# Optimization experiments

Measured on AMD Instinct MI355X. Metric: run time of the kernel, lower is better.

Reference implementation:

```python
import jax, jax.numpy as jnp
import numpy as np

B, S, D, H = 2, 2048, 2048, 16
HD = D // H  # head_dim = 128


def setup_inputs() -> dict:
    key = jax.random.key(0)
    k1, k2, k3, k4, k5, k6 = jax.random.split(key, 6)
    scale = 1.0 / np.sqrt(D)
    return {
        "hidden_states": jax.random.normal(k1, (B, S, D), dtype=jnp.float32),
        "attention_mask": jnp.ones((B, S), dtype=jnp.int32),
        "wq": jax.random.normal(k2, (D, D), dtype=jnp.float32) * scale,
        "wk": jax.random.normal(k3, (D, D), dtype=jnp.float32) * scale,
        "wv": jax.random.normal(k4, (D, D), dtype=jnp.float32) * scale,
        "wo": jax.random.normal(k5, (D, D), dtype=jnp.float32) * scale,
        "bo": jax.random.normal(k6, (D,), dtype=jnp.float32) * 0.01,
    }


def reference(hidden_states, attention_mask, wq, wk, wv, wo, bo):
    b, s, d = hidden_states.shape
    # QKV projections (no bias), split heads -> [B, S, H, HD]
    q = (hidden_states @ wq).reshape(b, s, H, HD)
    k = (hidden_states @ wk).reshape(b, s, H, HD)
    v = (hidden_states @ wv).reshape(b, s, H, HD)

    # combined causal + padding mask -> [B, 1, S, S]
    causal = jnp.tril(jnp.ones((s, s), dtype=bool))[None, None]
    pad = (attention_mask > 0)[:, None, None, :]  # [B,1,1,S]
    mask = jnp.logical_and(causal, pad)

    big_neg = jnp.finfo(hidden_states.dtype).min
    bias = jnp.where(mask, 0.0, big_neg).astype(hidden_states.dtype)

    # scaled dot-product attention (flax dot_product_attention scales by 1/sqrt(head_dim))
    scores = jnp.einsum("bqhd,bkhd->bhqk", q, k) / jnp.sqrt(jnp.asarray(HD, hidden_states.dtype))
    probs = jax.nn.softmax(scores + bias, axis=-1)
    ctx = jnp.einsum("bhqk,bkhd->bqhd", probs, v).reshape(b, s, d)

    return ctx @ wo + bo
```

## Files before the change

### kernel.cpp

```cpp
#include <hip/hip_runtime.h>
#include <hip/hip_bf16.h>
#include <stdint.h>

#define Bv 2
#define Sv 2048
#define Dv 2048
#define Hv 16
#define HDv 128
#define Mv (Bv*Sv)

typedef __attribute__((ext_vector_type(8))) short short8;
typedef __attribute__((ext_vector_type(4))) short short4v;
typedef __attribute__((ext_vector_type(4))) float f32x4;

__device__ __forceinline__ unsigned short bf16_rne(float f) {
    union { float f; uint32_t u; } c; c.f = f;
    uint32_t u = c.u;
    u += 0x7fffu + ((u >> 16) & 1u);
    return (unsigned short)(u >> 16);
}

__device__ __forceinline__ uint32_t cvt_pk_bf16(float lo, float hi) {
    uint32_t r;
    asm("v_cvt_pk_bf16_f32 %0, %1, %2" : "=v"(r) : "v"(lo), "v"(hi));
    return r;
}

__device__ __forceinline__ void gload16(const void* g, void* l) {
    __builtin_amdgcn_global_load_lds((const __attribute__((address_space(1))) void*)g,
                                     (__attribute__((address_space(3))) void*)l, 16, 0, 0);
}

__global__ void cvt_x_kernel(const float* __restrict__ x, unsigned short* __restrict__ xb) {
    int i = (blockIdx.x * 256 + threadIdx.x) * 4;
    float4 v = *(const float4*)(x + i);
    short4v o;
    o[0] = (short)bf16_rne(v.x);
    o[1] = (short)bf16_rne(v.y);
    o[2] = (short)bf16_rne(v.z);
    o[3] = (short)bf16_rne(v.w);
    *(short4v*)(xb + i) = o;
}

__global__ void cvt_wt_kernel(const float* __restrict__ w0, const float* __restrict__ w1,
                              const float* __restrict__ w2, const float* __restrict__ w3,
                              unsigned short* __restrict__ wt) {
    __shared__ unsigned short t[64][65];
    int z = blockIdx.z;
    const float* w = (z == 0) ? w0 : (z == 1) ? w1 : (z == 2) ? w2 : w3;
    unsigned short* o = wt + (size_t)z * Dv * Dv;
    int k0 = blockIdx.x * 64, n0 = blockIdx.y * 64;
    for (int i = threadIdx.x; i < 4096; i += 256) {
        int r = i >> 6, c = i & 63;
        t[r][c] = bf16_rne(w[(size_t)(k0 + r) * Dv + n0 + c]);
    }
    __syncthreads();
    for (int i = threadIdx.x; i < 4096; i += 256) {
        int r = i >> 6, c = i & 63;
        o[(size_t)(n0 + r) * Dv + k0 + c] = t[c][r];
    }
}

template<int FOUT>
__global__ __launch_bounds__(256) void gemm_bt_kernel(
    const unsigned short* __restrict__ A,
    const unsigned short* __restrict__ WtBase,
    unsigned short* __restrict__ CbBase,
    unsigned short* __restrict__ VTout,
    float* __restrict__ Cf,
    const float* __restrict__ bias)
{
    __shared__ unsigned short lA[128 * 32];
    __shared__ unsigned short lB[128 * 32];
    const int tid = threadIdx.x;
    const int wv = tid >> 6, ln = tid & 63;
    const int lr = ln & 15, lg = ln >> 4;
    const int wm = wv >> 1, wn = wv & 1;
    const int m0 = blockIdx.x * 128, n0 = blockIdx.y * 128;
    const int z = blockIdx.z;
    const unsigned short* Wt = WtBase + (size_t)z * Dv * Dv;
    unsigned short* Cb = CbBase + (size_t)z * (size_t)Mv * Dv;

    const int srow = tid >> 2;
    const int scol = (tid & 3) * 8;

    f32x4 acc[4][4];
    #pragma unroll
    for (int m = 0; m < 4; m++)
        #pragma unroll
        for (int n = 0; n < 4; n++)
            acc[m][n] = (f32x4){0.f, 0.f, 0.f, 0.f};

    for (int kt = 0; kt < Dv; kt += 32) {
        gload16(A  + (size_t)(m0 +      srow) * Dv + kt + scol, &lA[wv * 512]);
        gload16(A  + (size_t)(m0 + 64 + srow) * Dv + kt + scol, &lA[2048 + wv * 512]);
        gload16(Wt + (size_t)(n0 +      srow) * Dv + kt + scol, &lB[wv * 512]);
        gload16(Wt + (size_t)(n0 + 64 + srow) * Dv + kt + scol, &lB[2048 + wv * 512]);
        __syncthreads();

        short8 af[4], bfv[4];
        #pragma unroll
        for (int m = 0; m < 4; m++)
            af[m] = *(const short8*)&lA[(wm * 64 + m * 16 + lr) * 32 + lg * 8];
        #pragma unroll
        for (int n = 0; n < 4; n++)
            bfv[n] = *(const short8*)&lB[(wn * 64 + n * 16 + lr) * 32 + lg * 8];
        #pragma unroll
        for (int m = 0; m < 4; m++)
            #pragma unroll
            for (int n = 0; n < 4; n++)
                acc[m][n] = __builtin_amdgcn_mfma_f32_16x16x32_bf16(af[m], bfv[n], acc[m][n], 0, 0, 0);
        __syncthreads();
    }

    #pragma unroll
    for (int m = 0; m < 4; m++) {
        #pragma unroll
        for (int n = 0; n < 4; n++) {
            int row = m0 + wm * 64 + m * 16 + lg * 4;
            int col = n0 + wn * 64 + n * 16 + lr;
            if (FOUT) {
                #pragma unroll
                for (int r = 0; r < 4; r++)
                    Cf[(size_t)(row + r) * Dv + col] = acc[m][n][r] + bias[col];
            } else if (z == 2) {
                int bb = row >> 11, s = row & (Sv - 1);
                short4v o;
                #pragma unroll
                for (int r = 0; r < 4; r++) o[r] = (short)bf16_rne(acc[m][n][r]);
                *(short4v*)&VTout[((size_t)bb * Dv + col) * Sv + s] = o;
            } else {
                #pragma unroll
                for (int r = 0; r < 4; r++)
                    Cb[(size_t)(row + r) * Dv + col] = bf16_rne(acc[m][n][r]);
            }
        }
    }
}

__global__ __launch_bounds__(512) void attn_kernel(
    const unsigned short* __restrict__ Q, const unsigned short* __restrict__ K,
    const unsigned short* __restrict__ VT, const int* __restrict__ pmask,
    unsigned short* __restrict__ CTX)
{
    __shared__ unsigned short lK[2][64 * 128];
    __shared__ unsigned short lVt[2][128 * 64];
    __shared__ int lPmB[2][64];
    __shared__ int lPmOk[2];

    const int tid = threadIdx.x, wv = tid >> 6, ln = tid & 63;
    const int lr = ln & 15, lg = ln >> 4;
    const int L = blockIdx.x;
    const int bh = (L & 7) * 4 + ((L >> 3) & 3);
    const int b = bh >> 4, h = bh & 15;
    const int v = L >> 5;
    const int qidx = (v < 8) ? (15 - v) : (v - 8);
    const int q0 = qidx * 128;
    const int qw0 = q0 + wv * 16;
    const size_t hoff  = (size_t)b * Sv * Dv + (size_t)h * HDv;
    const size_t vtoff = ((size_t)b * Dv + (size_t)h * HDv) * Sv;

    short8 qf[4];
    #pragma unroll
    for (int ds = 0; ds < 4; ds++)
        qf[ds] = *(const short8*)&Q[hoff + (size_t)(qw0 + lr) * Dv + ds * 32 + lg * 8];

    size_t koff[2], voff[2];
    #pragma unroll
    for (int ii = 0; ii < 2; ++ii) {
        int slot = ii * 512 + wv * 64 + ln;
        int krow = slot >> 4, kch = slot & 15;
        koff[ii] = hoff + (size_t)krow * Dv + ((kch ^ (krow & 7)) << 3);
        int vrow = slot >> 3, vch = slot & 7;
        voff[ii] = vtoff + (size_t)vrow * Sv + ((vch ^ (vrow & 7)) << 3);
    }

    auto STAGE = [&](int t, int buf) {
        const size_t kadd = (size_t)(t << 6) * Dv;
        const int vadd = t << 6;
        unsigned short* kb = &lK[buf][0];
        unsigned short* vb = &lVt[buf][0];
        #pragma unroll
        for (int ii = 0; ii < 2; ++ii) {
            gload16(K + koff[ii] + kadd, kb + (ii * 512 + wv * 64) * 8);
            gload16(VT + voff[ii] + vadd, vb + (ii * 512 + wv * 64) * 8);
        }
        if (wv == 0) {
            int pmv = pmask[b * Sv + (t << 6) + ln];
            lPmB[buf][ln] = pmv;
            unsigned long long bal = __ballot(pmv != 0);
            if (ln == 0) lPmOk[buf] = (bal == ~0ull) ? 1 : 0;
        }
    };

    f32x4 acc[8];
    #pragma unroll
    for (int n = 0; n < 8; n++) acc[n] = (f32x4){0.f, 0.f, 0.f, 0.f};
    float mrow = -3.0e38f, lrow = 0.f;
    const float CS = 0.12751744f;
    const int qg = qw0 + lr;
    const int nt = (q0 >> 6) + 2;
    const int srcA = lr + ((lg & 1) << 5);
    const int srcB = srcA + 16;
    const bool hiSel = (lg >= 2);

    auto TILE = [&](int t, int buf, auto CAUSAL_c) {
        constexpr bool CAUSAL = decltype(CAUSAL_c)::value;
        const int kv0 = t << 6;
        const unsigned short* kb = &lK[buf][0];
        const unsigned short* vb = &lVt[buf][0];

        f32x4 st[4];
        #pragma unroll
        for (int t2 = 0; t2 < 4; ++t2) st[t2] = (f32x4){0.f, 0.f, 0.f, 0.f};
        __builtin_amdgcn_s_setprio(1);
        #pragma unroll
        for (int t2 = 0; t2 < 4; ++t2) {
            const int krow = t2 * 16 + lr;
            #pragma unroll
            for (int ds = 0; ds < 4; ++ds) {
                const int ch = ds * 4 + lg;
                short8 kf = *(const short8*)&kb[krow * 128 + ((ch ^ (krow & 7)) << 3)];
                st[t2] = __builtin_amdgcn_mfma_f32_16x16x32_bf16(kf, qf[ds], st[t2], 0, 0, 0);
            }
        }
        __builtin_amdgcn_s_setprio(0);

        float sv[4][4];
        float rmax;
        if constexpr (CAUSAL) {
            const int* pm = &lPmB[buf][0];
            #pragma unroll
            for (int t2 = 0; t2 < 4; ++t2)
                #pragma unroll
                for (int r = 0; r < 4; ++r) {
                    int kvl = t2 * 16 + lg * 4 + r;
                    bool ok = ((kv0 + kvl) <= qg) && (pm[kvl] != 0);
                    sv[t2][r] = ok ? st[t2][r] * CS : -1.0e30f;
                }
            rmax = sv[0][0];
            #pragma unroll
            for (int t2 = 0; t2 < 4; ++t2)
                #pragma unroll
                for (int r = 0; r < 4; ++r) rmax = fmaxf(rmax, sv[t2][r]);
            rmax = fmaxf(rmax, __shfl_xor(rmax, 16, 64));
            rmax = fmaxf(rmax, __shfl_xor(rmax, 32, 64));
        } else {
            rmax = st[0][0];
            #pragma unroll
            for (int t2 = 0; t2 < 4; ++t2)
                #pragma unroll
                for (int r = 0; r < 4; ++r) rmax = fmaxf(rmax, st[t2][r]);
            rmax = fmaxf(rmax, __shfl_xor(rmax, 16, 64));
            rmax = fmaxf(rmax, __shfl_xor(rmax, 32, 64));
            rmax *= CS;
        }

        if (!__all(rmax - mrow <= 8.0f)) {
            float mn = fmaxf(mrow, rmax);
            float alpha = exp2f(mrow - mn);
            mrow = mn;
            lrow *= alpha;
            #pragma unroll
            for (int n = 0; n < 8; n++)
                #pragma unroll
                for (int r = 0; r < 4; r++) acc[n][r] *= alpha;
        }

        float p[4][4]; float psum = 0.f;
        if constexpr (CAUSAL) {
            #pragma unroll
            for (int t2 = 0; t2 < 4; ++t2)
                #pragma unroll
                for (int r = 0; r < 4; ++r) {
                    float e = exp2f(sv[t2][r] - mrow);
                    p[t2][r] = (sv[t2][r] > -5.0e29f) ? e : 0.f;
                    psum += p[t2][r];
                }
        } else {
            if (lPmOk[buf]) {
                #pragma unroll
                for (int t2 = 0; t2 < 4; ++t2)
                    #pragma unroll
                    for (int r = 0; r < 4; ++r) {
                        p[t2][r] = exp2f(fmaf(st[t2][r], CS, -mrow));
                        psum += p[t2][r];
                    }
            } else {
                const int* pm = &lPmB[buf][0];
                #pragma unroll
                for (int t2 = 0; t2 < 4; ++t2)
                    #pragma unroll
                    for (int r = 0; r < 4; ++r) {
                        int kvl = t2 * 16 + lg * 4 + r;
                        float e = exp2f(fmaf(st[t2][r], CS, -mrow));
                        p[t2][r] = (pm[kvl] != 0) ? e : 0.f;
                        psum += p[t2][r];
                    }
            }
        }
        psum += __shfl_xor(psum, 16, 64);
        psum += __shfl_xor(psum, 32, 64);
        lrow += psum;

        uint32_t pk[4][2];
        #pragma unroll
        for (int t2 = 0; t2 < 4; ++t2)
            #pragma unroll
            for (int pp = 0; pp < 2; ++pp)
                pk[t2][pp] = cvt_pk_bf16(p[t2][2 * pp], p[t2][2 * pp + 1]);

        union U { uint32_t u[4]; short8 s; } pa0, pa1;
        {
            uint32_t l0 = (uint32_t)__shfl((int)pk[0][0], srcA, 64), h0 = (uint32_t)__shfl((int)pk[1][0], srcA, 64);
            uint32_t l1 = (uint32_t)__shfl((int)pk[0][1], srcA, 64), h1 = (uint32_t)__shfl((int)pk[1][1], srcA, 64);
            uint32_t l2 = (uint32_t)__shfl((int)pk[0][0], srcB, 64), h2 = (uint32_t)__shfl((int)pk[1][0], srcB, 64);
            uint32_t l3 = (uint32_t)__shfl((int)pk[0][1], srcB, 64), h3 = (uint32_t)__shfl((int)pk[1][1], srcB, 64);
            pa0.u[0] = hiSel ? h0 : l0; pa0.u[1] = hiSel ? h1 : l1;
            pa0.u[2] = hiSel ? h2 : l2; pa0.u[3] = hiSel ? h3 : l3;
        }
        {
            uint32_t l0 = (uint32_t)__shfl((int)pk[2][0], srcA, 64), h0 = (uint32_t)__shfl((int)pk[3][0], srcA, 64);
            uint32_t l1 = (uint32_t)__shfl((int)pk[2][1], srcA, 64), h1 = (uint32_t)__shfl((int)pk[3][1], srcA, 64);
            uint32_t l2 = (uint32_t)__shfl((int)pk[2][0], srcB, 64), h2 = (uint32_t)__shfl((int)pk[3][0], srcB, 64);
            uint32_t l3 = (uint32_t)__shfl((int)pk[2][1], srcB, 64), h3 = (uint32_t)__shfl((int)pk[3][1], srcB, 64);
            pa1.u[0] = hiSel ? h0 : l0; pa1.u[1] = hiSel ? h1 : l1;
            pa1.u[2] = hiSel ? h2 : l2; pa1.u[3] = hiSel ? h3 : l3;
        }

        __builtin_amdgcn_s_setprio(1);
        #pragma unroll
        for (int n = 0; n < 8; n++) {
            const int vrow = n * 16 + lr;
            short8 a0 = *(const short8*)&vb[vrow * 64 + ((lg ^ (vrow & 7)) << 3)];
            acc[n] = __builtin_amdgcn_mfma_f32_16x16x32_bf16(a0, pa0.s, acc[n], 0, 0, 0);
            short8 a1 = *(const short8*)&vb[vrow * 64 + (((4 + lg) ^ (vrow & 7)) << 3)];
            acc[n] = __builtin_amdgcn_mfma_f32_16x16x32_bf16(a1, pa1.s, acc[n], 0, 0, 0);
        }
        __builtin_amdgcn_s_setprio(0);
    };

    STAGE(0, 0);
    __syncthreads();
    int cur = 0;

    for (int t = 0; t < nt; ++t) {
        if (t + 1 < nt) STAGE(t + 1, cur ^ 1);
        const int kv0 = t << 6;
        if (kv0 <= qw0 + 15) {
            if (kv0 + 63 > qw0) TILE(t, cur, std::integral_constant<bool, true>{});
            else                TILE(t, cur, std::integral_constant<bool, false>{});
        }
        __syncthreads();
        cur ^= 1;
    }

    float inv = 1.0f / lrow;
    #pragma unroll
    for (int n = 0; n < 8; n++) {
        short4v o;
        #pragma unroll
        for (int r = 0; r < 4; r++) o[r] = (short)bf16_rne(acc[n][r] * inv);
        *(short4v*)&CTX[hoff + (size_t)qg * Dv + n * 16 + lg * 4] = o;
    }
}

extern "C" void kernel_launch(void* const* d_in, const int* in_sizes, int n_in,
                              void* d_out, int out_size, void* d_ws, size_t ws_size,
                              hipStream_t stream) {
    const float* hs  = (const float*)d_in[0];
    const int*   am  = (const int*)d_in[1];
    const float* wq  = (const float*)d_in[2];
    const float* wk  = (const float*)d_in[3];
    const float* wv_ = (const float*)d_in[4];
    const float* wo  = (const float*)d_in[5];
    const float* bo  = (const float*)d_in[6];
    float* out = (float*)d_out;

    char* ws = (char*)d_ws;
    unsigned short* Xb  = (unsigned short*)ws;
    unsigned short* Wt  = (unsigned short*)(ws + (size_t)16 * 1024 * 1024);
    unsigned short* QKV = (unsigned short*)(ws + (size_t)48 * 1024 * 1024);
    unsigned short* CTX = (unsigned short*)(ws + (size_t)96 * 1024 * 1024);
    unsigned short* VT  = QKV + 2 * (size_t)Mv * Dv;

    hipLaunchKernelGGL(cvt_x_kernel, dim3(Mv * Dv / 4 / 256), dim3(256), 0, stream, hs, Xb);
    hipLaunchKernelGGL(cvt_wt_kernel, dim3(32, 32, 4), dim3(256), 0, stream, wq, wk, wv_, wo, Wt);
    hipLaunchKernelGGL(gemm_bt_kernel<0>, dim3(32, 16, 3), dim3(256), 0, stream,
                       Xb, Wt, QKV, VT, (float*)nullptr, (const float*)nullptr);
    hipLaunchKernelGGL(attn_kernel, dim3(512), dim3(512), 0, stream,
                       QKV, QKV + (size_t)Mv * Dv, VT, am, CTX);
    hipLaunchKernelGGL(gemm_bt_kernel<1>, dim3(32, 16, 1), dim3(256), 0, stream,
                       CTX, Wt + 3 * (size_t)Dv * Dv, (unsigned short*)nullptr, (unsigned short*)nullptr, out, bo);
}
```

Before: 260.2 us.

## Replace GEMM with triple-buffered 128x256 tile kernel and separate V transpose

Replaces the simple 128x128 single-buffered GEMM with a 512-thread 128x256-tile kernel that uses 64-wide K steps and triple-buffered dynamic LDS with an XOR swizzle. Global loads for tile t+2 are issued while MFMAs run on tile t, with split barriers and setprio around the MFMA blocks. Blocks are mapped so each XCD owns a contiguous range of N columns. The fused V-transpose epilogue moves into a separate LDS-swizzled transpose kernel that writes into the reused X buffer. The aim is to hide memory latency and raise MFMA utilisation, at the cost of an extra kernel launch and an extra pass over V.

```diff
diff --git a/kernel.cpp b/kernel.cpp
--- a/kernel.cpp
+++ b/kernel.cpp
@@ -61,80 +61,168 @@
     }
 }
 
+__global__ void vt_kernel(const unsigned short* __restrict__ V, unsigned short* __restrict__ VT) {
+    __shared__ unsigned short t[64 * 64];
+    const int tid = threadIdx.x;
+    const int b = blockIdx.z;
+    const int s0 = blockIdx.x * 64, c0 = blockIdx.y * 64;
+    const unsigned short* Vb = V + (size_t)b * Sv * Dv;
+    unsigned short* VTb = VT + (size_t)b * Dv * Sv;
+    #pragma unroll
+    for (int ii = 0; ii < 2; ++ii) {
+        int i = tid + ii * 256;
+        int r = i >> 3, ch = i & 7;
+        short8 v = *(const short8*)&Vb[(size_t)(s0 + r) * Dv + c0 + ch * 8];
+        *(short8*)&t[r * 64 + ((ch ^ (r & 7)) << 3)] = v;
+    }
+    __syncthreads();
+    #pragma unroll
+    for (int ii = 0; ii < 2; ++ii) {
+        int o = tid + ii * 256;
+        int orow = o >> 3, och = o & 7;
+        short8 v;
+        #pragma unroll
+        for (int j = 0; j < 8; ++j) {
+            int r = och * 8 + j;
+            int c = orow;
+            v[j] = (short)t[r * 64 + ((((c >> 3) ^ (r & 7)) << 3) | (c & 7))];
+        }
+        *(short8*)&VTb[(size_t)(c0 + orow) * Sv + s0 + och * 8] = v;
+    }
+}
+
 template<int FOUT>
-__global__ __launch_bounds__(256) void gemm_bt_kernel(
+__global__ __launch_bounds__(512, 2) void gemm8_kernel(
     const unsigned short* __restrict__ A,
     const unsigned short* __restrict__ WtBase,
     unsigned short* __restrict__ CbBase,
-    unsigned short* __restrict__ VTout,
     float* __restrict__ Cf,
-    const float* __restrict__ bias)
+    const float* __restrict__ bias,
+    int per_xcd_n)
 {
-    __shared__ unsigned short lA[128 * 32];
-    __shared__ unsigned short lB[128 * 32];
+    extern __shared__ unsigned short lds[];
     const int tid = threadIdx.x;
     const int wv = tid >> 6, ln = tid & 63;
     const int lr = ln & 15, lg = ln >> 4;
-    const int wm = wv >> 1, wn = wv & 1;
-    const int m0 = blockIdx.x * 128, n0 = blockIdx.y * 128;
-    const int z = blockIdx.z;
-    const unsigned short* Wt = WtBase + (size_t)z * Dv * Dv;
-    unsigned short* Cb = CbBase + (size_t)z * (size_t)Mv * Dv;
-
-    const int srow = tid >> 2;
-    const int scol = (tid & 3) * 8;
+    const int wm = wv >> 2, wn = wv & 3;
+
+    const int bid = blockIdx.x;
+    const int xcd = bid & 7, idx = bid >> 3;
+    const int n_idx = xcd * per_xcd_n + (idx >> 5);
+    const int m_idx = idx & 31;
+    const int m0 = m_idx * 128;
+    const int n0g = n_idx * 256;
+    const int NT = Dv / 64;
+
+    const int srow = ln >> 3;
+    const int swz = ((ln & 7) ^ srow) << 3;
+    const unsigned short* Ab = A      + (size_t)(m0  + wv * 8 + srow) * Dv + swz;
+    const unsigned short* Bb = WtBase + (size_t)(n0g + wv * 8 + srow) * Dv + swz;
+
+    auto STAGE_A = [&](int t, int d) {
+        const unsigned short* g = Ab + t * 64;
+        #pragma unroll
+        for (int j = 0; j < 2; ++j)
+            gload16(g + (size_t)(j * 64) * Dv, &lds[d * 24576 + (j * 64 + wv * 8) * 64]);
+    };
+    auto STAGE_B = [&](int t, int d) {
+        const unsigned short* g = Bb + t * 64;
+        #pragma unroll
+        for (int j = 0; j < 4; ++j)
+            gload16(g + (size_t)(j * 64) * Dv, &lds[d * 24576 + 8192 + (j * 64 + wv * 8) * 64]);
+    };
+
+    const int aro = (wm * 64 + lr) * 64;
+    const int bro = (wn * 64 + lr) * 64;
+    const int ach0 = ((lg ^ (lr & 7)) << 3);
+    const int ach1 = (((4 + lg) ^ (lr & 7)) << 3);
 
     f32x4 acc[4][4];
     #pragma unroll
-    for (int m = 0; m < 4; m++)
-        #pragma unroll
-        for (int n = 0; n < 4; n++)
-            acc[m][n] = (f32x4){0.f, 0.f, 0.f, 0.f};
-
-    for (int kt = 0; kt < Dv; kt += 32) {
-        gload16(A  + (size_t)(m0 +      srow) * Dv + kt + scol, &lA[wv * 512]);
-        gload16(A  + (size_t)(m0 + 64 + srow) * Dv + kt + scol, &lA[2048 + wv * 512]);
-        gload16(Wt + (size_t)(n0 +      srow) * Dv + kt + scol, &lB[wv * 512]);
-        gload16(Wt + (size_t)(n0 + 64 + srow) * Dv + kt + scol, &lB[2048 + wv * 512]);
-        __syncthreads();
-
-        short8 af[4], bfv[4];
-        #pragma unroll
-        for (int m = 0; m < 4; m++)
-            af[m] = *(const short8*)&lA[(wm * 64 + m * 16 + lr) * 32 + lg * 8];
-        #pragma unroll
-        for (int n = 0; n < 4; n++)
-            bfv[n] = *(const short8*)&lB[(wn * 64 + n * 16 + lr) * 32 + lg * 8];
-        #pragma unroll
-        for (int m = 0; m < 4; m++)
-            #pragma unroll
-            for (int n = 0; n < 4; n++)
-                acc[m][n] = __builtin_amdgcn_mfma_f32_16x16x32_bf16(af[m], bfv[n], acc[m][n], 0, 0, 0);
-        __syncthreads();
-    }
-
-    #pragma unroll
-    for (int m = 0; m < 4; m++) {
-        #pragma unroll
-        for (int n = 0; n < 4; n++) {
-            int row = m0 + wm * 64 + m * 16 + lg * 4;
-            int col = n0 + wn * 64 + n * 16 + lr;
-            if (FOUT) {
+    for (int mi = 0; mi < 4; mi++)
+        #pragma unroll
+        for (int ni = 0; ni < 4; ni++)
+            acc[mi][ni] = (f32x4){0.f, 0.f, 0.f, 0.f};
+
+    STAGE_A(0, 0); STAGE_B(0, 0);
+    STAGE_A(1, 1); STAGE_B(1, 1);
+    asm volatile("s_waitcnt vmcnt(6)" ::: "memory");
+    asm volatile("s_barrier" ::: "memory");
+
+    for (int t = 0; t < NT; ++t) {
+        const int d = t % 3, d2 = (t + 2) % 3;
+        const unsigned short* la = &lds[d * 24576];
+        const unsigned short* lb = &lds[d * 24576 + 8192];
+
+        short8 af[4][2], bf0[2][2];
+        #pragma unroll
+        for (int mi = 0; mi < 4; mi++) {
+            af[mi][0] = *(const short8*)&la[aro + mi * 1024 + ach0];
+            af[mi][1] = *(const short8*)&la[aro + mi * 1024 + ach1];
+        }
+        #pragma unroll
+        for (int ni = 0; ni < 2; ni++) {
+            bf0[ni][0] = *(const short8*)&lb[bro + ni * 1024 + ach0];
+            bf0[ni][1] = *(const short8*)&lb[bro + ni * 1024 + ach1];
+        }
+        if (t + 2 < NT) STAGE_A(t + 2, d2);
+        asm volatile("s_barrier" ::: "memory");
+        __builtin_amdgcn_s_setprio(1);
+        #pragma unroll
+        for (int mi = 0; mi < 4; mi++)
+            #pragma unroll
+            for (int ni = 0; ni < 2; ni++) {
+                acc[mi][ni] = __builtin_amdgcn_mfma_f32_16x16x32_bf16(af[mi][0], bf0[ni][0], acc[mi][ni], 0, 0, 0);
+                acc[mi][ni] = __builtin_amdgcn_mfma_f32_16x16x32_bf16(af[mi][1], bf0[ni][1], acc[mi][ni], 0, 0, 0);
+            }
+        __builtin_amdgcn_s_setprio(0);
+
+        short8 bf1[2][2];
+        #pragma unroll
+        for (int ni = 0; ni < 2; ni++) {
+            bf1[ni][0] = *(const short8*)&lb[bro + (ni + 2) * 1024 + ach0];
+            bf1[ni][1] = *(const short8*)&lb[bro + (ni + 2) * 1024 + ach1];
+        }
+        if (t + 2 < NT) STAGE_B(t + 2, d2);
+        asm volatile("s_waitcnt vmcnt(6)" ::: "memory");
+        asm volatile("s_barrier" ::: "memory");
+        __builtin_amdgcn_s_setprio(1);
+        #pragma unroll
+        for (int mi = 0; mi < 4; mi++)
+            #pragma unroll
+            for (int ni = 0; ni < 2; ni++) {
+                acc[mi][ni + 2] = __builtin_amdgcn_mfma_f32_16x16x32_bf16(af[mi][0], bf1[ni][0], acc[mi][ni + 2], 0, 0, 0);
+                acc[mi][ni + 2] = __builtin_amdgcn_mfma_f32_16x16x32_bf16(af[mi][1], bf1[ni][1], acc[mi][ni + 2], 0, 0, 0);
+            }
+        __builtin_amdgcn_s_setprio(0);
+    }
+
+    if (FOUT) {
+        #pragma unroll
+        for (int mi = 0; mi < 4; mi++)
+            #pragma unroll
+            for (int ni = 0; ni < 4; ni++) {
+                int row = m0 + wm * 64 + mi * 16 + lg * 4;
+                int col = n0g + wn * 64 + ni * 16 + lr;
+                float bv = bias[col];
                 #pragma unroll
                 for (int r = 0; r < 4; r++)
-                    Cf[(size_t)(row + r) * Dv + col] = acc[m][n][r] + bias[col];
-            } else if (z == 2) {
-                int bb = row >> 11, s = row & (Sv - 1);
-                short4v o;
-                #pragma unroll
-                for (int r = 0; r < 4; r++) o[r] = (short)bf16_rne(acc[m][n][r]);
-                *(short4v*)&VTout[((size_t)bb * Dv + col) * Sv + s] = o;
-            } else {
+                    Cf[(size_t)(row + r) * Dv + col] = acc[mi][ni][r] + bv;
+            }
+    } else {
+        const int z = n0g >> 11;
+        unsigned short* Cz = CbBase + (size_t)z * Mv * Dv;
+        const int ncl = (n0g & 2047) + wn * 64;
+        #pragma unroll
+        for (int mi = 0; mi < 4; mi++)
+            #pragma unroll
+            for (int ni = 0; ni < 4; ni++) {
+                int row = m0 + wm * 64 + mi * 16 + lg * 4;
+                int col = ncl + ni * 16 + lr;
                 #pragma unroll
                 for (int r = 0; r < 4; r++)
-                    Cb[(size_t)(row + r) * Dv + col] = bf16_rne(acc[m][n][r]);
-            }
-        }
+                    Cz[(size_t)(row + r) * Dv + col] = bf16_rne(acc[mi][ni][r]);
+            }
     }
 }
 
@@ -382,14 +470,24 @@
     unsigned short* Wt  = (unsigned short*)(ws + (size_t)16 * 1024 * 1024);
     unsigned short* QKV = (unsigned short*)(ws + (size_t)48 * 1024 * 1024);
     unsigned short* CTX = (unsigned short*)(ws + (size_t)96 * 1024 * 1024);
-    unsigned short* VT  = QKV + 2 * (size_t)Mv * Dv;
+    unsigned short* VT  = Xb;
+
+    const int LDSB = 3 * 24576 * 2;
+    static bool attrSet = false;
+    if (!attrSet) {
+        hipFuncSetAttribute((const void*)gemm8_kernel<0>, hipFuncAttributeMaxDynamicSharedMemorySize, LDSB);
+        hipFuncSetAttribute((const void*)gemm8_kernel<1>, hipFuncAttributeMaxDynamicSharedMemorySize, LDSB);
+        attrSet = true;
+    }
 
     hipLaunchKernelGGL(cvt_x_kernel, dim3(Mv * Dv / 4 / 256), dim3(256), 0, stream, hs, Xb);
     hipLaunchKernelGGL(cvt_wt_kernel, dim3(32, 32, 4), dim3(256), 0, stream, wq, wk, wv_, wo, Wt);
-    hipLaunchKernelGGL(gemm_bt_kernel<0>, dim3(32, 16, 3), dim3(256), 0, stream,
-                       Xb, Wt, QKV, VT, (float*)nullptr, (const float*)nullptr);
+    hipLaunchKernelGGL(gemm8_kernel<0>, dim3(768), dim3(512), LDSB, stream,
+                       Xb, Wt, QKV, (float*)nullptr, (const float*)nullptr, 3);
+    hipLaunchKernelGGL(vt_kernel, dim3(32, 32, 2), dim3(256), 0, stream,
+                       QKV + 2 * (size_t)Mv * Dv, VT);
     hipLaunchKernelGGL(attn_kernel, dim3(512), dim3(512), 0, stream,
                        QKV, QKV + (size_t)Mv * Dv, VT, am, CTX);
-    hipLaunchKernelGGL(gemm_bt_kernel<1>, dim3(32, 16, 1), dim3(256), 0, stream,
-                       CTX, Wt + 3 * (size_t)Dv * Dv, (unsigned short*)nullptr, (unsigned short*)nullptr, out, bo);
-}
+    hipLaunchKernelGGL(gemm8_kernel<1>, dim3(256), dim3(512), LDSB, stream,
+                       CTX, Wt + 3 * (size_t)Dv * Dv, (unsigned short*)nullptr, out, bo, 1);
+}
```

After: 243.1 us. -6.6%, faster.
